# Optimization experiments

Measured on AMD Instinct MI355X. Metric: run time of the kernel, lower is better.

## Reference

```python
import jax, jax.numpy as jnp
import numpy as np

TOP_K = 48
NUM_RBF = 16
NUM_RBF_SC = 8
MAXREL = 32
EDGE_F = 128
EPS_D = 1e-6
LN_EPS = 1e-5


def gather_nodes(nodes, idx):
    # nodes: [B, L, C], idx: [B, L, K] -> [B, L, K, C]
    return jax.vmap(lambda n, i: n[i])(nodes, idx)


def rbf(D, count):
    # D: [..., ] -> [..., count]; mu in [2, 22], sigma = 20/count
    mu = jnp.linspace(2.0, 22.0, count)
    sigma = (22.0 - 2.0) / count
    return jnp.exp(-(((D[..., None] - mu) / sigma) ** 2))


def layer_norm(x, g, b):
    mu = jnp.mean(x, -1, keepdims=True)
    var = jnp.mean((x - mu) ** 2, -1, keepdims=True)
    return g * (x - mu) / jnp.sqrt(var + LN_EPS) + b


def setup_inputs() -> dict:
    key = jax.random.key(0)
    ks = jax.random.split(key, 8)
    B, Lr = 1, 1024
    X = jax.random.normal(ks[0], (B, Lr, 37, 3), dtype=jnp.float32)
    mask = jnp.ones((B, Lr), dtype=jnp.float32)
    atom_mask = jnp.ones((B, Lr, 37), dtype=jnp.float32)
    residue_idx = jnp.arange(B * Lr, dtype=jnp.int64 if jax.config.jax_enable_x64 else jnp.int32).reshape(B, Lr)
    dihedral_mask = jnp.ones((B, Lr), dtype=jnp.float32)
    chain_labels = jnp.zeros((B, Lr), dtype=jnp.int32)
    W_pos = jax.random.normal(ks[1], (16, 2 * MAXREL + 2), dtype=jnp.float32) * 0.1
    b_pos = jnp.zeros((16,), dtype=jnp.float32)
    W_e = jax.random.normal(ks[2], (EDGE_F, 16 + NUM_RBF * 25), dtype=jnp.float32) * 0.05
    g_e = jnp.ones((EDGE_F,), dtype=jnp.float32)
    be_e = jnp.zeros((EDGE_F,), dtype=jnp.float32)
    W_s = jax.random.normal(ks[3], (EDGE_F, NUM_RBF_SC * 32 * 5), dtype=jnp.float32) * 0.05
    g_s = jnp.ones((EDGE_F,), dtype=jnp.float32)
    b_s = jnp.zeros((EDGE_F,), dtype=jnp.float32)
    return {"X": X, "L": 1024, "mask": mask, "atom_mask": atom_mask,
            "residue_idx": residue_idx, "dihedral_mask": dihedral_mask,
            "chain_labels": chain_labels, "W_pos": W_pos, "b_pos": b_pos,
            "W_e": W_e, "g_e": g_e, "be_e": be_e, "W_s": W_s, "g_s": g_s, "b_s": b_s}


def reference(X, L, mask, atom_mask, residue_idx, dihedral_mask, chain_labels,
              W_pos, b_pos, W_e, g_e, be_e, W_s, g_s, b_s):
    # Virtual Cb from ideal geometry
    b_v = X[:, :, 1, :] - X[:, :, 0, :]
    c_v = X[:, :, 2, :] - X[:, :, 1, :]
    a_v = jnp.cross(b_v, c_v)
    Cb = -0.58273431 * a_v + 0.56802827 * b_v - 0.54067466 * c_v + X[:, :, 1, :]
    Ca = X[:, :, 1, :]
    N = X[:, :, 0, :]
    C = X[:, :, 2, :]
    O = X[:, :, 4, :]

    # _dist: masked pairwise Ca distances + top-k smallest
    mask2d = mask[:, None, :] * mask[:, :, None]  # [B, L, L]
    dX = Ca[:, :, None, :] - Ca[:, None, :, :]
    D = mask2d * jnp.sqrt(jnp.sum(dX ** 2, -1) + EPS_D)
    D_max = jnp.max(D, -1, keepdims=True)
    D_adj = D + (1.0 - mask2d) * D_max
    neg_vals, E_idx = jax.lax.top_k(-D_adj, TOP_K)
    D_neighbors = -neg_vals  # [B, L, K]

    coords = {'N': N, 'Ca': Ca, 'C': C, 'O': O, 'Cb': Cb}
    pairs = [('N','N'),('C','C'),('O','O'),('Cb','Cb'),('Ca','N'),('Ca','C'),('Ca','O'),
             ('Ca','Cb'),('N','C'),('N','O'),('N','Cb'),('Cb','C'),('Cb','O'),('O','C'),
             ('N','Ca'),('C','Ca'),('O','Ca'),('Cb','Ca'),('C','N'),('O','N'),('Cb','N'),
             ('C','Cb'),('O','Cb'),('C','O')]
    A_st = jnp.stack([coords[a] for a, _ in pairs])  # [24, B, L, 3]
    B_st = jnp.stack([coords[b] for _, b in pairs])
    B_nb = jax.vmap(gather_nodes, (0, None))(B_st, E_idx)  # [24, B, L, K, 3]
    Dp = jnp.sqrt(jnp.sum((A_st[:, :, :, None, :] - B_nb) ** 2, -1) + EPS_D)  # [24,B,L,K]
    RBF_pairs = rbf(Dp, NUM_RBF)  # [24, B, L, K, 16]
    Bt, Lr, K = E_idx.shape
    RBF_pairs = jnp.moveaxis(RBF_pairs, 0, 3).reshape(Bt, Lr, K, 24 * NUM_RBF)
    RBF_all = jnp.concatenate([rbf(D_neighbors, NUM_RBF), RBF_pairs], -1)  # [B,L,K,400]

    # Positional encodings
    ri_nb = gather_nodes(residue_idx[..., None], E_idx)[..., 0]  # [B,L,K]
    offset = residue_idx[:, :, None] - ri_nb
    ch_nb = gather_nodes(chain_labels[..., None], E_idx)[..., 0]
    E_chains = (chain_labels[:, :, None] - ch_nb == 0).astype(jnp.int32)
    d = jnp.clip(offset + MAXREL, 0, 2 * MAXREL) * E_chains + (1 - E_chains) * (2 * MAXREL + 1)
    d_onehot = jax.nn.one_hot(d, 2 * MAXREL + 2, dtype=jnp.float32)
    E_positional = d_onehot @ W_pos.T + b_pos
    E = jnp.concatenate([E_positional, RBF_all], -1)  # [B,L,K,416]

    # Sidechain RBFs on the first min(100, K) neighbors
    Ks = min(100, K)
    E_idx_sub = E_idx[:, :, :Ks]
    am_g = gather_nodes(atom_mask, E_idx_sub)  # [B,L,Ks,37]
    S = X[:, :, 5:37, :]  # [B,L,32,3]
    S_nb = gather_nodes(S.reshape(Bt, Lr, 32 * 3), E_idx_sub).reshape(Bt, Lr, Ks, 32, 3)
    anchors = jnp.stack([N, Ca, C, O, Cb], 2)  # [B,L,5,3], anchor order matches loop order
    Ds = jnp.sqrt(jnp.sum((anchors[:, :, None, :, None, :] - S_nb[:, :, :, None, :, :]) ** 2, -1) + EPS_D)
    # Ds: [B,L,Ks,5,32]; rbf_side -> [B,L,Ks,5,32,8]; masked by neighbor atom mask
    RBF_s = rbf(Ds, NUM_RBF_SC) * am_g[:, :, :, None, 5:37, None]
    E_s = RBF_s.reshape(Bt, Lr, Ks, 5 * 32 * NUM_RBF_SC)  # [B,L,Ks,1280]

    E_s = layer_norm(E_s @ W_s.T, g_s, b_s)
    E = layer_norm(E @ W_e.T, g_e, be_e)
    return (E, E_idx, E_s, E_idx_sub)
```

## Files before the change

### kernel.cpp

```cpp
#include <hip/hip_runtime.h>
#include <math.h>

#define LRES 1024
#define TOPK 48
#define NEDGE (LRES*TOPK)

typedef short short8 __attribute__((ext_vector_type(8)));
typedef float f32x4  __attribute__((ext_vector_type(4)));

#define OUT_E     0
#define OUT_EIDX  6291456
#define OUT_ES    6340608
#define OUT_EIDX2 12632064

#define WS_COORDS 0
#define WS_DNB    15360
#define WS_EIDX   64512
#define WS_WPE    113664
#define WS_WPS    140288

#define DE 1.06666667f
#define QE 0.10273976f
#define DS 1.14285714f
#define QS 0.07337053f

__constant__ int PA[24] = {0,2,3,4,1,1,1,1,0,0,0,4,4,3,0,2,3,4,2,3,4,2,3,2};
__constant__ int PB[24] = {0,2,3,4,0,2,3,4,2,3,4,2,3,2,1,1,1,1,0,0,0,4,4,3};

__device__ inline short f2bf(float f) {
    unsigned u = __float_as_uint(f);
    unsigned r = (u + 0x7FFFu + ((u >> 16) & 1u)) >> 16;
    return (short)r;
}

__device__ inline short8 pack8(const float* fv) {
    union { short8 s; unsigned u[4]; } r;
    #pragma unroll
    for (int i = 0; i < 4; ++i)
        r.u[i] = __builtin_amdgcn_perm(__float_as_uint(fv[2*i+1]),
                                       __float_as_uint(fv[2*i]), 0x07060302u);
    return r.s;
}

__global__ __launch_bounds__(256) void k_pre(const float* __restrict__ X,
                                             const float* __restrict__ mask,
                                             const float* __restrict__ We,
                                             const float* __restrict__ Ws,
                                             float* __restrict__ coords,
                                             short* __restrict__ WpE,
                                             short* __restrict__ WpS,
                                             float* __restrict__ Dnb,
                                             int* __restrict__ Eidx,
                                             float* __restrict__ out) {
    int blk = blockIdx.x, t = threadIdx.x;
    if (blk < 256) {
        __shared__ float sCa[LRES*3];
        __shared__ float sM[LRES];
        for (int j = t; j < LRES; j += 256) {
            sCa[j*3+0] = X[j*111 + 3];
            sCa[j*3+1] = X[j*111 + 4];
            sCa[j*3+2] = X[j*111 + 5];
            sM[j] = mask[j];
        }
        __syncthreads();
        int w = t >> 6, lane = t & 63;
        int i = blk * 4 + w;
        float cx = sCa[i*3], cy = sCa[i*3+1], cz = sCa[i*3+2];
        float mi = sM[i];
        float dv[16], m2v[16];
        float lmax = -1e30f;
        #pragma unroll
        for (int s = 0; s < 16; ++s) {
            int j = s*64 + lane;
            float dx = cx - sCa[j*3], dy = cy - sCa[j*3+1], dz = cz - sCa[j*3+2];
            float d  = __builtin_amdgcn_sqrtf(dx*dx + dy*dy + dz*dz + 1e-6f);
            float m2 = mi * sM[j];
            dv[s] = m2 * d; m2v[s] = m2;
            lmax = fmaxf(lmax, dv[s]);
        }
        #pragma unroll
        for (int off = 32; off; off >>= 1) lmax = fmaxf(lmax, __shfl_xor(lmax, off));
        unsigned long long key[16];
        unsigned long long mkey = ~0ull; int mslot = 0;
        #pragma unroll
        for (int s = 0; s < 16; ++s) {
            float dadj = dv[s] + (1.0f - m2v[s]) * lmax;
            key[s] = (((unsigned long long)__float_as_uint(dadj)) << 10) | (unsigned)(s*64 + lane);
            if (key[s] < mkey) { mkey = key[s]; mslot = s; }
        }
        for (int it = 0; it < TOPK; ++it) {
            unsigned long long wk = mkey;
            #pragma unroll
            for (int off = 32; off; off >>= 1) {
                unsigned long long o = __shfl_xor(wk, off);
                wk = (o < wk) ? o : wk;
            }
            if (lane == 0) {
                int j = (int)(wk & 1023u);
                int id = i*TOPK + it;
                Dnb[id]  = __uint_as_float((unsigned)(wk >> 10));
                Eidx[id] = j;
                out[OUT_EIDX  + id] = (float)j;
                out[OUT_EIDX2 + id] = (float)j;
            }
            if (mkey == wk) {
                key[mslot] = ~0ull;
                mkey = ~0ull;
                #pragma unroll
                for (int s = 0; s < 16; ++s)
                    if (key[s] < mkey) { mkey = key[s]; mslot = s; }
            }
        }
    } else if (blk < 896) {
        int g = (blk - 256) * 256 + t;
        if (g < 8*13*64*8) {
            int j = g & 7, lane = (g >> 3) & 63, gg = g >> 9;
            int ks = gg % 13, nt = gg / 13;
            int n = nt*16 + (lane & 15), k = ks*32 + (lane >> 4)*8 + j;
            WpE[g] = f2bf(We[n*416 + k]);
        }
        if (g < 8*40*64*8) {
            int j = g & 7, lane = (g >> 3) & 63, gg = g >> 9;
            int ks = gg % 40, nt = gg / 40;
            int n = nt*16 + (lane & 15), k = ks*32 + (lane >> 4)*8 + j;
            WpS[g] = f2bf(Ws[n*1280 + k]);
        }
    } else {
        int r = (blk - 896) * 256 + t;
        if (r >= LRES) return;
        const float* xr = X + r * 111;
        float N[3], Ca[3], C[3], O[3], bv[3], cv[3], av[3];
        #pragma unroll
        for (int d = 0; d < 3; ++d) {
            N[d]  = xr[0*3 + d];  Ca[d] = xr[1*3 + d];
            C[d]  = xr[2*3 + d];  O[d]  = xr[4*3 + d];
            bv[d] = Ca[d] - N[d]; cv[d] = C[d] - Ca[d];
        }
        av[0] = bv[1]*cv[2] - bv[2]*cv[1];
        av[1] = bv[2]*cv[0] - bv[0]*cv[2];
        av[2] = bv[0]*cv[1] - bv[1]*cv[0];
        float* o = coords + r * 15;
        #pragma unroll
        for (int d = 0; d < 3; ++d) {
            float Cb = -0.58273431f*av[d] + 0.56802827f*bv[d] - 0.54067466f*cv[d] + Ca[d];
            o[0*3+d] = N[d]; o[1*3+d] = Ca[d]; o[2*3+d] = C[d];
            o[3*3+d] = O[d]; o[4*3+d] = Cb;
        }
    }
}

__global__ __launch_bounds__(256, 2) void k_edge(const float* __restrict__ coords,
                                                 const float* __restrict__ X,
                                                 const float* __restrict__ amask,
                                                 const short* __restrict__ WpE,
                                                 const short* __restrict__ WpS,
                                                 const float* __restrict__ Dnb,
                                                 const int* __restrict__ Eidx,
                                                 const int* __restrict__ ri,
                                                 const int* __restrict__ ch,
                                                 const float* __restrict__ Wpos,
                                                 const float* __restrict__ bpos,
                                                 const float* __restrict__ ge,
                                                 const float* __restrict__ be,
                                                 const float* __restrict__ gs,
                                                 const float* __restrict__ bs,
                                                 float* __restrict__ out) {
    __shared__ float smem[5808];
    int t = threadIdx.x;
    int w = t >> 6, lane = t & 63, quad = lane >> 4, l16 = lane & 15;

    if (blockIdx.x < 1536) {
        float* u_hbuf = smem;
        float* sA3    = smem + 4224;
        float* part   = smem + 4272;
        float* part2  = smem + 4528;
        float* smu    = smem + 4784;
        float* srs    = smem + 4816;
        int id0 = blockIdx.x * 32;
        int i0 = id0 / TOPK;

        if (t < 45) {
            int rr = i0 + t / 15;
            if (rr > LRES-1) rr = LRES-1;
            sA3[t] = coords[rr*15 + t%15];
        }
        int s1 = 4*w + quad;
        float S[2][2][3], am[2][2];
        int im[2];
        #pragma unroll
        for (int mt = 0; mt < 2; ++mt) {
            int id = id0 + mt*16 + l16;
            int j  = Eidx[id];
            im[mt] = id / TOPK;
            const float* xp = X + (j*37 + 5)*3;
            const float* ap = amask + j*37 + 5;
            #pragma unroll
            for (int h = 0; h < 2; ++h) {
                int s = s1 + h*16;
                S[mt][h][0] = xp[s*3+0];
                S[mt][h][1] = xp[s*3+1];
                S[mt][h][2] = xp[s*3+2];
                am[mt][h]   = ap[s];
            }
        }
        __syncthreads();

        f32x4 acc[2][8] = {};
        const short8* bp = (const short8*)WpS;

        for (int a = 0; a < 5; ++a) {
            float A[2][3];
            #pragma unroll
            for (int mt = 0; mt < 2; ++mt) {
                int base = (im[mt] - i0)*15 + a*3;
                A[mt][0] = sA3[base+0];
                A[mt][1] = sA3[base+1];
                A[mt][2] = sA3[base+2];
            }
            #pragma unroll
            for (int h = 0; h < 2; ++h) {
                int ks = a*8 + w + h*4;
                short8 afrag[2];
                #pragma unroll
                for (int mt = 0; mt < 2; ++mt) {
                    float dx = A[mt][0] - S[mt][h][0];
                    float dy = A[mt][1] - S[mt][h][1];
                    float dz = A[mt][2] - S[mt][h][2];
                    float d  = __builtin_amdgcn_sqrtf(fmaf(dz,dz,fmaf(dy,dy,fmaf(dx,dx,1e-6f))));
                    float u  = fmaf(d, 0.4f, -0.8f);
                    float e0 = __expf(-u*u) * am[mt][h];
                    float g  = __expf(fmaf(2.0f*DS, u, -DS*DS));
                    float fv[8];
                    fv[0] = e0;
                    #pragma unroll
                    for (int r = 1; r < 8; ++r) { e0 *= g; g *= QS; fv[r] = e0; }
                    afrag[mt] = pack8(fv);
                }
                #pragma unroll
                for (int nt = 0; nt < 8; ++nt) {
                    short8 b = bp[(nt*40 + ks)*64 + lane];
                    acc[0][nt] = __builtin_amdgcn_mfma_f32_16x16x32_bf16(afrag[0], b, acc[0][nt], 0,0,0);
                    acc[1][nt] = __builtin_amdgcn_mfma_f32_16x16x32_bf16(afrag[1], b, acc[1][nt], 0,0,0);
                }
            }
        }

        float* hbuf = u_hbuf;
        __syncthreads();
        for (int ww = 0; ww < 4; ++ww) {
            if (w == ww) {
                #pragma unroll
                for (int mt = 0; mt < 2; ++mt)
                #pragma unroll
                for (int nt = 0; nt < 8; ++nt)
                #pragma unroll
                for (int r = 0; r < 4; ++r) {
                    int e = mt*16 + quad*4 + r;
                    float* p = &hbuf[e*132 + nt*16 + l16];
                    if (ww == 0) *p = acc[mt][nt][r]; else *p += acc[mt][nt][r];
                }
            }
            __syncthreads();
        }
        {
            int e = t >> 3, p = t & 7;
            float s = 0.f, s2 = 0.f;
            #pragma unroll
            for (int q = 0; q < 16; ++q) {
                float x = hbuf[e*132 + p*16 + q];
                s += x; s2 += x*x;
            }
            part[e*8+p] = s; part2[e*8+p] = s2;
        }
        __syncthreads();
        if (t < 32) {
            float s = 0.f, s2 = 0.f;
            #pragma unroll
            for (int p = 0; p < 8; ++p) { s += part[t*8+p]; s2 += part2[t*8+p]; }
            float mu = s * (1.0f/128.0f);
            float var = s2 * (1.0f/128.0f) - mu*mu;
            smu[t] = mu; srs[t] = rsqrtf(var + 1e-5f);
        }
        __syncthreads();
        for (int it = t; it < 32*128; it += 256) {
            int e = it >> 7, f = it & 127;
            float x = hbuf[e*132 + f];
            out[OUT_ES + (size_t)(id0 + e)*128 + f] = gs[f] * (x - smu[e]) * srs[e] + bs[f];
        }
    } else {
        float* sA     = smem;
        float* sB     = smem + 480;
        float* u_hbuf = smem + 960;
        float* part   = smem + 5184;
        float* part2  = smem + 5440;
        float* smu    = smem + 5696;
        float* srs    = smem + 5728;
        int*   sdpos  = (int*)(smem + 5760);
        float* sdist  = u_hbuf;
        float* sposf  = u_hbuf + 32*27;
        int id0 = (blockIdx.x - 1536) * 32;

        if (t < 32) {
            int id = id0 + t, i = id / TOPK, j = Eidx[id];
            int off = ri[i] - ri[j];
            sdpos[t] = (ch[i] == ch[j]) ? min(max(off + 32, 0), 64) : 65;
            sdist[t*27] = Dnb[id];
        }
        for (int it = t; it < 32*15; it += 256) {
            int e = it / 15, q = it % 15;
            int id = id0 + e, i = id / TOPK, j = Eidx[id];
            sA[e*15+q] = coords[i*15+q];
            sB[e*15+q] = coords[j*15+q];
        }
        __syncthreads();
        for (int it = t; it < 32*24; it += 256) {
            int e = it / 24, p = it % 24, a = PA[p], b = PB[p];
            float dx = sA[e*15+a*3+0] - sB[e*15+b*3+0];
            float dy = sA[e*15+a*3+1] - sB[e*15+b*3+1];
            float dz = sA[e*15+a*3+2] - sB[e*15+b*3+2];
            sdist[e*27 + 1 + p] = __builtin_amdgcn_sqrtf(dx*dx + dy*dy + dz*dz + 1e-6f);
        }
        for (int it = t; it < 32*16; it += 256) {
            int e = it >> 4, c = it & 15;
            sposf[e*17 + c] = Wpos[c*66 + sdpos[e]] + bpos[c];
        }
        __syncthreads();

        f32x4 acc[2][8] = {};
        const short8* bp = (const short8*)WpE;
        float rb = (quad & 1) ? 8.0f*DE : 0.0f;

        for (int ks = w; ks < 13; ks += 4) {
            short8 afrag[2];
            #pragma unroll
            for (int mt = 0; mt < 2; ++mt) {
                int e = mt*16 + l16;
                float fv[8];
                if (ks == 0 && quad < 2) {
                    #pragma unroll
                    for (int j = 0; j < 8; ++j) fv[j] = sposf[e*17 + quad*8 + j];
                } else {
                    int p = (ks == 0) ? 0 : (2*ks - 1 + (quad >> 1));
                    float d = sdist[e*27 + p];
                    float u = fmaf(d, 0.8f, -1.6f) - rb;
                    float e0 = __expf(-u*u);
                    float g  = __expf(fmaf(2.0f*DE, u, -DE*DE));
                    fv[0] = e0;
                    #pragma unroll
                    for (int r = 1; r < 8; ++r) { e0 *= g; g *= QE; fv[r] = e0; }
                }
                afrag[mt] = pack8(fv);
            }
            #pragma unroll
            for (int nt = 0; nt < 8; ++nt) {
                short8 b = bp[(nt*13 + ks)*64 + lane];
                acc[0][nt] = __builtin_amdgcn_mfma_f32_16x16x32_bf16(afrag[0], b, acc[0][nt], 0,0,0);
                acc[1][nt] = __builtin_amdgcn_mfma_f32_16x16x32_bf16(afrag[1], b, acc[1][nt], 0,0,0);
            }
        }

        float* hbuf = u_hbuf;
        __syncthreads();
        for (int ww = 0; ww < 4; ++ww) {
            if (w == ww) {
                #pragma unroll
                for (int mt = 0; mt < 2; ++mt)
                #pragma unroll
                for (int nt = 0; nt < 8; ++nt)
                #pragma unroll
                for (int r = 0; r < 4; ++r) {
                    int e = mt*16 + quad*4 + r;
                    float* p = &hbuf[e*132 + nt*16 + l16];
                    if (ww == 0) *p = acc[mt][nt][r]; else *p += acc[mt][nt][r];
                }
            }
            __syncthreads();
        }
        {
            int e = t >> 3, p = t & 7;
            float s = 0.f, s2 = 0.f;
            #pragma unroll
            for (int q = 0; q < 16; ++q) {
                float x = hbuf[e*132 + p*16 + q];
                s += x; s2 += x*x;
            }
            part[e*8+p] = s; part2[e*8+p] = s2;
        }
        __syncthreads();
        if (t < 32) {
            float s = 0.f, s2 = 0.f;
            #pragma unroll
            for (int p = 0; p < 8; ++p) { s += part[t*8+p]; s2 += part2[t*8+p]; }
            float mu = s * (1.0f/128.0f);
            float var = s2 * (1.0f/128.0f) - mu*mu;
            smu[t] = mu; srs[t] = rsqrtf(var + 1e-5f);
        }
        __syncthreads();
        for (int it = t; it < 32*128; it += 256) {
            int e = it >> 7, f = it & 127;
            float x = hbuf[e*132 + f];
            out[OUT_E + (size_t)(id0 + e)*128 + f] = ge[f] * (x - smu[e]) * srs[e] + be[f];
        }
    }
}

extern "C" void kernel_launch(void* const* d_in, const int* in_sizes, int n_in,
                              void* d_out, int out_size, void* d_ws, size_t ws_size,
                              hipStream_t stream) {
    (void)in_sizes; (void)n_in; (void)out_size; (void)ws_size;
    const float* X     = (const float*)d_in[0];
    const float* mask  = (const float*)d_in[2];
    const float* amask = (const float*)d_in[3];
    const int*   ri    = (const int*)d_in[4];
    const int*   ch    = (const int*)d_in[6];
    const float* Wpos  = (const float*)d_in[7];
    const float* bpos  = (const float*)d_in[8];
    const float* We    = (const float*)d_in[9];
    const float* ge    = (const float*)d_in[10];
    const float* be    = (const float*)d_in[11];
    const float* Ws    = (const float*)d_in[12];
    const float* gs    = (const float*)d_in[13];
    const float* bs    = (const float*)d_in[14];

    float* out    = (float*)d_out;
    float* ws     = (float*)d_ws;
    float* coords = ws + WS_COORDS;
    float* Dnb    = ws + WS_DNB;
    int*   Eidx   = (int*)(ws + WS_EIDX);
    short* WpE    = (short*)(ws + WS_WPE);
    short* WpS    = (short*)(ws + WS_WPS);

    k_pre <<<dim3(900),  dim3(256), 0, stream>>>(X, mask, We, Ws, coords,
                                                 WpE, WpS, Dnb, Eidx, out);
    k_edge<<<dim3(3072), dim3(256), 0, stream>>>(coords, X, amask, WpE, WpS,
                                                 Dnb, Eidx, ri, ch, Wpos, bpos,
                                                 ge, be, gs, bs, out);
}
```

Measured before the change: 187.4 us.

## Split edges across waves instead of K, fuse LayerNorm in registers

The edge kernel changes its work split. Each wave now owns 32 full edges and loops over the whole reduction dimension, where before the four waves split K and reduced through shared memory with a serialized accumulate loop. Each block now covers 128 edges with 768 blocks instead of 3072, and LayerNorm is done from the MFMA accumulators with cross-lane shuffles and written straight to global memory. The packed weight layout is reordered so a K-step's eight N-tiles are contiguous. This removes the shared-memory reduction and many barriers, in exchange for more registers per thread (8 sidechain coords per edge) and fewer blocks in flight.

After: 315.1 us. 68.2% more time.

```diff
diff --git a/kernel.cpp b/kernel.cpp
--- a/kernel.cpp
+++ b/kernel.cpp
@@ -40,6 +40,28 @@
         r.u[i] = __builtin_amdgcn_perm(__float_as_uint(fv[2*i+1]),
                                        __float_as_uint(fv[2*i]), 0x07060302u);
     return r.s;
+}
+
+__device__ __forceinline__ void ln_write(const f32x4* acc, float* op,
+                                         const float* gv, const float* bv,
+                                         int l16, int quad) {
+    #pragma unroll
+    for (int r = 0; r < 4; ++r) {
+        float s = 0.f, s2 = 0.f;
+        #pragma unroll
+        for (int nt = 0; nt < 8; ++nt) { float x = acc[nt][r]; s += x; s2 = fmaf(x, x, s2); }
+        #pragma unroll
+        for (int m = 1; m <= 8; m <<= 1) {
+            s  += __shfl_xor(s,  m);
+            s2 += __shfl_xor(s2, m);
+        }
+        float mu = s * 0.0078125f;
+        float rs = rsqrtf(fmaf(s2, 0.0078125f, -mu*mu) + 1e-5f);
+        float* row = op + (quad*4 + r)*128 + l16;
+        #pragma unroll
+        for (int nt = 0; nt < 8; ++nt)
+            row[nt*16] = gv[nt]*(acc[nt][r] - mu)*rs + bv[nt];
+    }
 }
 
 __global__ __launch_bounds__(256) void k_pre(const float* __restrict__ X,
@@ -113,15 +135,15 @@
         }
     } else if (blk < 896) {
         int g = (blk - 256) * 256 + t;
-        if (g < 8*13*64*8) {
+        if (g < 104*512) {
             int j = g & 7, lane = (g >> 3) & 63, gg = g >> 9;
-            int ks = gg % 13, nt = gg / 13;
+            int nt = gg & 7, ks = gg >> 3;
             int n = nt*16 + (lane & 15), k = ks*32 + (lane >> 4)*8 + j;
             WpE[g] = f2bf(We[n*416 + k]);
         }
-        if (g < 8*40*64*8) {
+        if (g < 320*512) {
             int j = g & 7, lane = (g >> 3) & 63, gg = g >> 9;
-            int ks = gg % 40, nt = gg / 40;
+            int nt = gg & 7, ks = gg >> 3;
             int n = nt*16 + (lane & 15), k = ks*32 + (lane >> 4)*8 + j;
             WpS[g] = f2bf(Ws[n*1280 + k]);
         }
@@ -165,176 +187,128 @@
                                                  const float* __restrict__ gs,
                                                  const float* __restrict__ bs,
                                                  float* __restrict__ out) {
-    __shared__ float smem[5808];
+    __shared__ float smem[7744];
     int t = threadIdx.x;
     int w = t >> 6, lane = t & 63, quad = lane >> 4, l16 = lane & 15;
-
-    if (blockIdx.x < 1536) {
-        float* u_hbuf = smem;
-        float* sA3    = smem + 4224;
-        float* part   = smem + 4272;
-        float* part2  = smem + 4528;
-        float* smu    = smem + 4784;
-        float* srs    = smem + 4816;
-        int id0 = blockIdx.x * 32;
-        int i0 = id0 / TOPK;
-
-        if (t < 45) {
-            int rr = i0 + t / 15;
-            if (rr > LRES-1) rr = LRES-1;
-            sA3[t] = coords[rr*15 + t%15];
-        }
-        int s1 = 4*w + quad;
-        float S[2][2][3], am[2][2];
-        int im[2];
+    int bid = blockIdx.x >> 1;
+    int idB = bid * 128;
+    int i0  = idB / TOPK;
+
+    if (!(blockIdx.x & 1)) {
+        float* sA = smem;
+        if (t < 60) {
+            int rr = i0 + t/15; if (rr > LRES-1) rr = LRES-1;
+            sA[t] = coords[rr*15 + t%15];
+        }
+        int id0 = idB + w*32;
+        int ro[2];
+        float S[2][8][3], am[2][8];
         #pragma unroll
         for (int mt = 0; mt < 2; ++mt) {
             int id = id0 + mt*16 + l16;
             int j  = Eidx[id];
-            im[mt] = id / TOPK;
+            ro[mt] = (id/TOPK - i0)*15;
             const float* xp = X + (j*37 + 5)*3;
             const float* ap = amask + j*37 + 5;
             #pragma unroll
-            for (int h = 0; h < 2; ++h) {
-                int s = s1 + h*16;
-                S[mt][h][0] = xp[s*3+0];
-                S[mt][h][1] = xp[s*3+1];
-                S[mt][h][2] = xp[s*3+2];
-                am[mt][h]   = ap[s];
+            for (int q = 0; q < 8; ++q) {
+                int s = q*4 + quad;
+                S[mt][q][0] = xp[s*3+0];
+                S[mt][q][1] = xp[s*3+1];
+                S[mt][q][2] = xp[s*3+2];
+                am[mt][q]   = ap[s];
             }
         }
         __syncthreads();
 
         f32x4 acc[2][8] = {};
-        const short8* bp = (const short8*)WpS;
-
+        const short8* bw = (const short8*)WpS + lane;
         for (int a = 0; a < 5; ++a) {
             float A[2][3];
             #pragma unroll
             for (int mt = 0; mt < 2; ++mt) {
-                int base = (im[mt] - i0)*15 + a*3;
-                A[mt][0] = sA3[base+0];
-                A[mt][1] = sA3[base+1];
-                A[mt][2] = sA3[base+2];
-            }
-            #pragma unroll
-            for (int h = 0; h < 2; ++h) {
-                int ks = a*8 + w + h*4;
-                short8 afrag[2];
+                A[mt][0] = sA[ro[mt] + a*3 + 0];
+                A[mt][1] = sA[ro[mt] + a*3 + 1];
+                A[mt][2] = sA[ro[mt] + a*3 + 2];
+            }
+            #pragma unroll
+            for (int q = 0; q < 8; ++q) {
+                int ks = a*8 + q;
+                short8 af[2];
                 #pragma unroll
                 for (int mt = 0; mt < 2; ++mt) {
-                    float dx = A[mt][0] - S[mt][h][0];
-                    float dy = A[mt][1] - S[mt][h][1];
-                    float dz = A[mt][2] - S[mt][h][2];
+                    float dx = A[mt][0] - S[mt][q][0];
+                    float dy = A[mt][1] - S[mt][q][1];
+                    float dz = A[mt][2] - S[mt][q][2];
                     float d  = __builtin_amdgcn_sqrtf(fmaf(dz,dz,fmaf(dy,dy,fmaf(dx,dx,1e-6f))));
                     float u  = fmaf(d, 0.4f, -0.8f);
-                    float e0 = __expf(-u*u) * am[mt][h];
+                    float e0 = __expf(-u*u) * am[mt][q];
                     float g  = __expf(fmaf(2.0f*DS, u, -DS*DS));
                     float fv[8];
                     fv[0] = e0;
                     #pragma unroll
                     for (int r = 1; r < 8; ++r) { e0 *= g; g *= QS; fv[r] = e0; }
-                    afrag[mt] = pack8(fv);
+                    af[mt] = pack8(fv);
                 }
                 #pragma unroll
                 for (int nt = 0; nt < 8; ++nt) {
-                    short8 b = bp[(nt*40 + ks)*64 + lane];
-                    acc[0][nt] = __builtin_amdgcn_mfma_f32_16x16x32_bf16(afrag[0], b, acc[0][nt], 0,0,0);
-                    acc[1][nt] = __builtin_amdgcn_mfma_f32_16x16x32_bf16(afrag[1], b, acc[1][nt], 0,0,0);
+                    short8 b = bw[ks*512 + nt*64];
+                    acc[0][nt] = __builtin_amdgcn_mfma_f32_16x16x32_bf16(af[0], b, acc[0][nt], 0,0,0);
+                    acc[1][nt] = __builtin_amdgcn_mfma_f32_16x16x32_bf16(af[1], b, acc[1][nt], 0,0,0);
                 }
             }
         }
-
-        float* hbuf = u_hbuf;
-        __syncthreads();
-        for (int ww = 0; ww < 4; ++ww) {
-            if (w == ww) {
-                #pragma unroll
-                for (int mt = 0; mt < 2; ++mt)
-                #pragma unroll
-                for (int nt = 0; nt < 8; ++nt)
-                #pragma unroll
-                for (int r = 0; r < 4; ++r) {
-                    int e = mt*16 + quad*4 + r;
-                    float* p = &hbuf[e*132 + nt*16 + l16];
-                    if (ww == 0) *p = acc[mt][nt][r]; else *p += acc[mt][nt][r];
-                }
-            }
-            __syncthreads();
-        }
-        {
-            int e = t >> 3, p = t & 7;
-            float s = 0.f, s2 = 0.f;
-            #pragma unroll
-            for (int q = 0; q < 16; ++q) {
-                float x = hbuf[e*132 + p*16 + q];
-                s += x; s2 += x*x;
-            }
-            part[e*8+p] = s; part2[e*8+p] = s2;
-        }
-        __syncthreads();
-        if (t < 32) {
-            float s = 0.f, s2 = 0.f;
-            #pragma unroll
-            for (int p = 0; p < 8; ++p) { s += part[t*8+p]; s2 += part2[t*8+p]; }
-            float mu = s * (1.0f/128.0f);
-            float var = s2 * (1.0f/128.0f) - mu*mu;
-            smu[t] = mu; srs[t] = rsqrtf(var + 1e-5f);
-        }
-        __syncthreads();
-        for (int it = t; it < 32*128; it += 256) {
-            int e = it >> 7, f = it & 127;
-            float x = hbuf[e*132 + f];
-            out[OUT_ES + (size_t)(id0 + e)*128 + f] = gs[f] * (x - smu[e]) * srs[e] + bs[f];
-        }
+        float gv[8], bv[8];
+        #pragma unroll
+        for (int nt = 0; nt < 8; ++nt) { gv[nt] = gs[nt*16+l16]; bv[nt] = bs[nt*16+l16]; }
+        #pragma unroll
+        for (int mt = 0; mt < 2; ++mt)
+            ln_write(acc[mt], out + OUT_ES + (size_t)(id0 + mt*16)*128, gv, bv, l16, quad);
     } else {
-        float* sA     = smem;
-        float* sB     = smem + 480;
-        float* u_hbuf = smem + 960;
-        float* part   = smem + 5184;
-        float* part2  = smem + 5440;
-        float* smu    = smem + 5696;
-        float* srs    = smem + 5728;
-        int*   sdpos  = (int*)(smem + 5760);
-        float* sdist  = u_hbuf;
-        float* sposf  = u_hbuf + 32*27;
-        int id0 = (blockIdx.x - 1536) * 32;
-
-        if (t < 32) {
-            int id = id0 + t, i = id / TOPK, j = Eidx[id];
+        float* sA    = smem;
+        float* sB    = smem + 64;
+        float* sdist = smem + 1984;
+        float* sposf = smem + 5440;
+        int*   sdpos = (int*)(smem + 7616);
+
+        if (t < 60) {
+            int rr = i0 + t/15; if (rr > LRES-1) rr = LRES-1;
+            sA[t] = coords[rr*15 + t%15];
+        }
+        if (t < 128) {
+            int id = idB + t, i = id/TOPK, j = Eidx[id];
             int off = ri[i] - ri[j];
             sdpos[t] = (ch[i] == ch[j]) ? min(max(off + 32, 0), 64) : 65;
             sdist[t*27] = Dnb[id];
         }
-        for (int it = t; it < 32*15; it += 256) {
-            int e = it / 15, q = it % 15;
-            int id = id0 + e, i = id / TOPK, j = Eidx[id];
-            sA[e*15+q] = coords[i*15+q];
+        for (int it = t; it < 128*15; it += 256) {
+            int e = it/15, q = it%15;
+            int j = Eidx[idB + e];
             sB[e*15+q] = coords[j*15+q];
         }
         __syncthreads();
-        for (int it = t; it < 32*24; it += 256) {
-            int e = it / 24, p = it % 24, a = PA[p], b = PB[p];
-            float dx = sA[e*15+a*3+0] - sB[e*15+b*3+0];
-            float dy = sA[e*15+a*3+1] - sB[e*15+b*3+1];
-            float dz = sA[e*15+a*3+2] - sB[e*15+b*3+2];
+        for (int it = t; it < 128*24; it += 256) {
+            int e = it/24, p = it%24, pa = PA[p], pb = PB[p];
+            int roe = ((idB+e)/TOPK - i0)*15;
+            float dx = sA[roe+pa*3+0] - sB[e*15+pb*3+0];
+            float dy = sA[roe+pa*3+1] - sB[e*15+pb*3+1];
+            float dz = sA[roe+pa*3+2] - sB[e*15+pb*3+2];
             sdist[e*27 + 1 + p] = __builtin_amdgcn_sqrtf(dx*dx + dy*dy + dz*dz + 1e-6f);
         }
-        for (int it = t; it < 32*16; it += 256) {
+        for (int it = t; it < 128*16; it += 256) {
             int e = it >> 4, c = it & 15;
             sposf[e*17 + c] = Wpos[c*66 + sdpos[e]] + bpos[c];
         }
         __syncthreads();
 
         f32x4 acc[2][8] = {};
-        const short8* bp = (const short8*)WpE;
+        const short8* bw = (const short8*)WpE + lane;
         float rb = (quad & 1) ? 8.0f*DE : 0.0f;
-
-        for (int ks = w; ks < 13; ks += 4) {
-            short8 afrag[2];
+        for (int ks = 0; ks < 13; ++ks) {
+            short8 af[2];
             #pragma unroll
             for (int mt = 0; mt < 2; ++mt) {
-                int e = mt*16 + l16;
+                int e = w*32 + mt*16 + l16;
                 float fv[8];
                 if (ks == 0 && quad < 2) {
                     #pragma unroll
@@ -349,58 +323,22 @@
                     #pragma unroll
                     for (int r = 1; r < 8; ++r) { e0 *= g; g *= QE; fv[r] = e0; }
                 }
-                afrag[mt] = pack8(fv);
+                af[mt] = pack8(fv);
             }
             #pragma unroll
             for (int nt = 0; nt < 8; ++nt) {
-                short8 b = bp[(nt*13 + ks)*64 + lane];
-                acc[0][nt] = __builtin_amdgcn_mfma_f32_16x16x32_bf16(afrag[0], b, acc[0][nt], 0,0,0);
-                acc[1][nt] = __builtin_amdgcn_mfma_f32_16x16x32_bf16(afrag[1], b, acc[1][nt], 0,0,0);
-            }
-        }
-
-        float* hbuf = u_hbuf;
-        __syncthreads();
-        for (int ww = 0; ww < 4; ++ww) {
-            if (w == ww) {
-                #pragma unroll
-                for (int mt = 0; mt < 2; ++mt)
-                #pragma unroll
-                for (int nt = 0; nt < 8; ++nt)
-                #pragma unroll
-                for (int r = 0; r < 4; ++r) {
-                    int e = mt*16 + quad*4 + r;
-                    float* p = &hbuf[e*132 + nt*16 + l16];
-                    if (ww == 0) *p = acc[mt][nt][r]; else *p += acc[mt][nt][r];
-                }
-            }
-            __syncthreads();
-        }
-        {
-            int e = t >> 3, p = t & 7;
-            float s = 0.f, s2 = 0.f;
-            #pragma unroll
-            for (int q = 0; q < 16; ++q) {
-                float x = hbuf[e*132 + p*16 + q];
-                s += x; s2 += x*x;
-            }
-            part[e*8+p] = s; part2[e*8+p] = s2;
-        }
-        __syncthreads();
-        if (t < 32) {
-            float s = 0.f, s2 = 0.f;
-            #pragma unroll
-            for (int p = 0; p < 8; ++p) { s += part[t*8+p]; s2 += part2[t*8+p]; }
-            float mu = s * (1.0f/128.0f);
-            float var = s2 * (1.0f/128.0f) - mu*mu;
-            smu[t] = mu; srs[t] = rsqrtf(var + 1e-5f);
-        }
-        __syncthreads();
-        for (int it = t; it < 32*128; it += 256) {
-            int e = it >> 7, f = it & 127;
-            float x = hbuf[e*132 + f];
-            out[OUT_E + (size_t)(id0 + e)*128 + f] = ge[f] * (x - smu[e]) * srs[e] + be[f];
-        }
+                short8 b = bw[ks*512 + nt*64];
+                acc[0][nt] = __builtin_amdgcn_mfma_f32_16x16x32_bf16(af[0], b, acc[0][nt], 0,0,0);
+                acc[1][nt] = __builtin_amdgcn_mfma_f32_16x16x32_bf16(af[1], b, acc[1][nt], 0,0,0);
+            }
+        }
+        int id0 = idB + w*32;
+        float gv[8], bv[8];
+        #pragma unroll
+        for (int nt = 0; nt < 8; ++nt) { gv[nt] = ge[nt*16+l16]; bv[nt] = be[nt*16+l16]; }
+        #pragma unroll
+        for (int mt = 0; mt < 2; ++mt)
+            ln_write(acc[mt], out + OUT_E + (size_t)(id0 + mt*16)*128, gv, bv, l16, quad);
     }
 }
 
@@ -430,9 +368,9 @@
     short* WpE    = (short*)(ws + WS_WPE);
     short* WpS    = (short*)(ws + WS_WPS);
 
-    k_pre <<<dim3(900),  dim3(256), 0, stream>>>(X, mask, We, Ws, coords,
-                                                 WpE, WpS, Dnb, Eidx, out);
-    k_edge<<<dim3(3072), dim3(256), 0, stream>>>(coords, X, amask, WpE, WpS,
-                                                 Dnb, Eidx, ri, ch, Wpos, bpos,
-                                                 ge, be, gs, bs, out);
-}
+    k_pre <<<dim3(900), dim3(256), 0, stream>>>(X, mask, We, Ws, coords,
+                                                WpE, WpS, Dnb, Eidx, out);
+    k_edge<<<dim3(768), dim3(256), 0, stream>>>(coords, X, amask, WpE, WpS,
+                                                Dnb, Eidx, ri, ch, Wpos, bpos,
+                                                ge, be, gs, bs, out);
+}
```

## Replace serialized cross-wave accumulation with per-wave buffers and shuffle-based LayerNorm

Applied to the files above, without the earlier changes.

The old epilogue had each of the four waves take turns adding its MFMA partial sums into one shared buffer, with a barrier per wave, and then reduced LayerNorm statistics in two shared-memory passes. The new helper gives each wave its own shared buffer, sums the four buffers on read, and computes mean and variance with warp shuffles, one 16-row half at a time. Outputs are written with nontemporal stores. This cuts barriers and serial LDS work, but shared memory grows from about 23 KB to about 38 KB per block, which could limit occupancy.

Result: faster. 182.9 us (-2.4%).

```diff
diff --git a/kernel.cpp b/kernel.cpp
--- a/kernel.cpp
+++ b/kernel.cpp
@@ -40,6 +40,46 @@
         r.u[i] = __builtin_amdgcn_perm(__float_as_uint(fv[2*i+1]),
                                        __float_as_uint(fv[2*i]), 0x07060302u);
     return r.s;
+}
+
+__device__ __forceinline__ void kred_ln(const f32x4 (*acc)[8], float* hb,
+                                        float* outp, const float* g,
+                                        const float* b, int t, int w,
+                                        int quad, int l16) {
+    int e = t >> 4, c = t & 15;
+    float gv[8], bv[8];
+    #pragma unroll
+    for (int k = 0; k < 8; ++k) { gv[k] = g[c + 16*k]; bv[k] = b[c + 16*k]; }
+    float* hw = hb + w*2144;
+    #pragma unroll
+    for (int mt = 0; mt < 2; ++mt) {
+        __syncthreads();
+        #pragma unroll
+        for (int nt = 0; nt < 8; ++nt)
+        #pragma unroll
+        for (int r = 0; r < 4; ++r)
+            hw[(quad*4 + r)*134 + nt*16 + l16] = acc[mt][nt][r];
+        __syncthreads();
+        float s = 0.f, s2 = 0.f, vals[8];
+        #pragma unroll
+        for (int k = 0; k < 8; ++k) {
+            int col = e*134 + c + 16*k;
+            float v = hb[col] + hb[2144 + col] + hb[4288 + col] + hb[6432 + col];
+            vals[k] = v; s += v; s2 = fmaf(v, v, s2);
+        }
+        #pragma unroll
+        for (int m = 1; m <= 8; m <<= 1) {
+            s  += __shfl_xor(s,  m);
+            s2 += __shfl_xor(s2, m);
+        }
+        float mu = s * 0.0078125f;
+        float rs = rsqrtf(fmaf(s2, 0.0078125f, -mu*mu) + 1e-5f);
+        float* row = outp + (size_t)(mt*16 + e)*128 + c;
+        #pragma unroll
+        for (int k = 0; k < 8; ++k)
+            __builtin_nontemporal_store(gv[k]*(vals[k] - mu)*rs + bv[k],
+                                        &row[16*k]);
+    }
 }
 
 __global__ __launch_bounds__(256) void k_pre(const float* __restrict__ X,
@@ -165,17 +205,13 @@
                                                  const float* __restrict__ gs,
                                                  const float* __restrict__ bs,
                                                  float* __restrict__ out) {
-    __shared__ float smem[5808];
+    __shared__ float smem[9536];
     int t = threadIdx.x;
     int w = t >> 6, lane = t & 63, quad = lane >> 4, l16 = lane & 15;
+    float* hb = smem;
 
     if (blockIdx.x < 1536) {
-        float* u_hbuf = smem;
-        float* sA3    = smem + 4224;
-        float* part   = smem + 4272;
-        float* part2  = smem + 4528;
-        float* smu    = smem + 4784;
-        float* srs    = smem + 4816;
+        float* sA3 = smem + 8576;
         int id0 = blockIdx.x * 32;
         int i0 = id0 / TOPK;
 
@@ -244,60 +280,13 @@
                 }
             }
         }
-
-        float* hbuf = u_hbuf;
-        __syncthreads();
-        for (int ww = 0; ww < 4; ++ww) {
-            if (w == ww) {
-                #pragma unroll
-                for (int mt = 0; mt < 2; ++mt)
-                #pragma unroll
-                for (int nt = 0; nt < 8; ++nt)
-                #pragma unroll
-                for (int r = 0; r < 4; ++r) {
-                    int e = mt*16 + quad*4 + r;
-                    float* p = &hbuf[e*132 + nt*16 + l16];
-                    if (ww == 0) *p = acc[mt][nt][r]; else *p += acc[mt][nt][r];
-                }
-            }
-            __syncthreads();
-        }
-        {
-            int e = t >> 3, p = t & 7;
-            float s = 0.f, s2 = 0.f;
-            #pragma unroll
-            for (int q = 0; q < 16; ++q) {
-                float x = hbuf[e*132 + p*16 + q];
-                s += x; s2 += x*x;
-            }
-            part[e*8+p] = s; part2[e*8+p] = s2;
-        }
-        __syncthreads();
-        if (t < 32) {
-            float s = 0.f, s2 = 0.f;
-            #pragma unroll
-            for (int p = 0; p < 8; ++p) { s += part[t*8+p]; s2 += part2[t*8+p]; }
-            float mu = s * (1.0f/128.0f);
-            float var = s2 * (1.0f/128.0f) - mu*mu;
-            smu[t] = mu; srs[t] = rsqrtf(var + 1e-5f);
-        }
-        __syncthreads();
-        for (int it = t; it < 32*128; it += 256) {
-            int e = it >> 7, f = it & 127;
-            float x = hbuf[e*132 + f];
-            out[OUT_ES + (size_t)(id0 + e)*128 + f] = gs[f] * (x - smu[e]) * srs[e] + bs[f];
-        }
+        kred_ln(acc, hb, out + OUT_ES + (size_t)id0*128, gs, bs, t, w, quad, l16);
     } else {
-        float* sA     = smem;
-        float* sB     = smem + 480;
-        float* u_hbuf = smem + 960;
-        float* part   = smem + 5184;
-        float* part2  = smem + 5440;
-        float* smu    = smem + 5696;
-        float* srs    = smem + 5728;
-        int*   sdpos  = (int*)(smem + 5760);
-        float* sdist  = u_hbuf;
-        float* sposf  = u_hbuf + 32*27;
+        float* sA    = smem + 8576;
+        float* sB    = smem + 9056;
+        float* sdist = hb;
+        float* sposf = hb + 864;
+        int*   sdpos = (int*)(hb + 1408);
         int id0 = (blockIdx.x - 1536) * 32;
 
         if (t < 32) {
@@ -358,49 +347,7 @@
                 acc[1][nt] = __builtin_amdgcn_mfma_f32_16x16x32_bf16(afrag[1], b, acc[1][nt], 0,0,0);
             }
         }
-
-        float* hbuf = u_hbuf;
-        __syncthreads();
-        for (int ww = 0; ww < 4; ++ww) {
-            if (w == ww) {
-                #pragma unroll
-                for (int mt = 0; mt < 2; ++mt)
-                #pragma unroll
-                for (int nt = 0; nt < 8; ++nt)
-                #pragma unroll
-                for (int r = 0; r < 4; ++r) {
-                    int e = mt*16 + quad*4 + r;
-                    float* p = &hbuf[e*132 + nt*16 + l16];
-                    if (ww == 0) *p = acc[mt][nt][r]; else *p += acc[mt][nt][r];
-                }
-            }
-            __syncthreads();
-        }
-        {
-            int e = t >> 3, p = t & 7;
-            float s = 0.f, s2 = 0.f;
-            #pragma unroll
-            for (int q = 0; q < 16; ++q) {
-                float x = hbuf[e*132 + p*16 + q];
-                s += x; s2 += x*x;
-            }
-            part[e*8+p] = s; part2[e*8+p] = s2;
-        }
-        __syncthreads();
-        if (t < 32) {
-            float s = 0.f, s2 = 0.f;
-            #pragma unroll
-            for (int p = 0; p < 8; ++p) { s += part[t*8+p]; s2 += part2[t*8+p]; }
-            float mu = s * (1.0f/128.0f);
-            float var = s2 * (1.0f/128.0f) - mu*mu;
-            smu[t] = mu; srs[t] = rsqrtf(var + 1e-5f);
-        }
-        __syncthreads();
-        for (int it = t; it < 32*128; it += 256) {
-            int e = it >> 7, f = it & 127;
-            float x = hbuf[e*132 + f];
-            out[OUT_E + (size_t)(id0 + e)*128 + f] = ge[f] * (x - smu[e]) * srs[e] + be[f];
-        }
+        kred_ln(acc, hb, out + OUT_E + (size_t)id0*128, ge, be, t, w, quad, l16);
     }
 }
 
```
